# Performance work log

Measured on AMD Instinct MI355X. Metric: run time of the kernel, lower is better.

The kernel has to match this reference:

```python
import jax, jax.numpy as jnp
import numpy as np

EPS = 1e-6

def _sigma(x):
    # ELU+1 feature map used by Infini-Attention / linear attention
    return jax.nn.elu(x) + 1.0

def setup_inputs() -> dict:
    key = jax.random.key(0)
    ks = jax.random.split(key, 8)
    B, S, H, D = 2, 4096, 2048, 128
    sc = 1.0 / np.sqrt(H)
    return {
        "hidden_states": jax.random.normal(ks[0], (B, S, H), jnp.float32),
        "w_q": jax.random.normal(ks[1], (D, H), jnp.float32) * sc,
        "w_k": jax.random.normal(ks[2], (D, H), jnp.float32) * sc,
        "w_v": jax.random.normal(ks[3], (D, H), jnp.float32) * sc,
        "w_o": jax.random.normal(ks[4], (H, D), jnp.float32) * (1.0 / np.sqrt(D)),
        "gate": jnp.zeros((1,), jnp.float32),
        "M": jax.random.normal(ks[5], (D, D), jnp.float32),
        "z": jax.random.uniform(ks[6], (D,), jnp.float32) + 0.5,
    }

def reference(hidden_states, w_q, w_k, w_v, w_o, gate, M, z):
    # projections (torch Linear: x @ W^T)
    q = jnp.einsum('bsh,dh->bsd', hidden_states, w_q)
    k = jnp.einsum('bsh,dh->bsd', hidden_states, w_k)
    v = jnp.einsum('bsh,dh->bsd', hidden_states, w_v)

    # --- compressive memory retrieve: sigma(q) M / (sigma(q) . z) ---
    sq = _sigma(q)                                   # [B,S,D]
    mem_num = jnp.einsum('bsd,de->bse', sq, M)       # [B,S,D]
    mem_den = jnp.einsum('bsd,d->bs', sq, z) + EPS
    memory_output = mem_num / mem_den[..., None]

    # --- causal linear attention (cumulative-sum, non-softmax) ---
    pq, pk = _sigma(q), _sigma(k)
    kv_cum = jnp.cumsum(jnp.einsum('bsd,bse->bsde', pk, v), axis=1)  # [B,S,D,D] running state
    k_cum = jnp.cumsum(pk, axis=1)                                    # [B,S,D]
    num = jnp.einsum('bsd,bsde->bse', pq, kv_cum)
    den = jnp.einsum('bsd,bsd->bs', pq, k_cum) + EPS
    local_output = num / den[..., None]

    g = jax.nn.sigmoid(gate)                         # [1], broadcasts
    output = g * memory_output + (1.0 - g) * local_output

    # --- delta-rule memory update ---
    sk = _sigma(k)
    v_ret = jnp.einsum('bsd,de->bse', sk, M) / (jnp.einsum('bsd,d->bs', sk, z) + EPS)[..., None]
    M_new = M + jnp.einsum('bsd,bse->de', sk, v - v_ret)
    z_new = z + jnp.sum(sk, axis=(0, 1))

    out = jnp.einsum('bsd,hd->bsh', output, w_o)
    return out, M_new, z_new
```

## Files before the change

kernel.cpp:

```cpp
#include <hip/hip_runtime.h>
#include <hip/hip_bf16.h>
#include <math.h>

#define DI __device__ __forceinline__

typedef __bf16 bf16x8 __attribute__((ext_vector_type(8)));
typedef float  f32x4  __attribute__((ext_vector_type(4)));

static constexpr int   Bsz  = 2, Ssz = 4096, Hsz = 2048, Dsz = 128;
static constexpr int   Nrow = Bsz * Ssz;
static constexpr int   NCH  = Nrow / 128;
static constexpr int   CPB  = Ssz / 128;
static constexpr int   WN   = Dsz * Hsz;
static constexpr float EPSF = 1e-6f;

static constexpr size_t WQKV_OFF = 0;
static constexpr size_t WO_OFF   = (size_t)3*WN*2;
static constexpr size_t MB_OFF   = WO_OFF + (size_t)WN*2;
static constexpr size_t MBT_OFF  = MB_OFF + 32768;
static constexpr size_t QB_OFF   = MBT_OFF + 32768;
static constexpr size_t KB_OFF   = QB_OFF + (size_t)Nrow*Dsz*2;
static constexpr size_t VB_OFF   = KB_OFF + (size_t)Nrow*Dsz*2;
static constexpr size_t PB_OFF   = VB_OFF + (size_t)Nrow*Dsz*2;
static constexpr size_t ACC_OFF  = PB_OFF + (size_t)Nrow*Dsz*2;
static constexpr size_t KVT_OFF  = ACC_OFF;
static constexpr size_t KVTP_OFF = ACC_OFF + (size_t)4*1024*1024;
static constexpr size_t MPART_OFF= ACC_OFF + (size_t)6*1024*1024;
static constexpr size_t KSUM_OFF = ACC_OFF + (size_t)10*1024*1024;
static constexpr size_t KPRE_OFF = KSUM_OFF + 32768;

DI float b2f(unsigned short u) {
    union { float f; unsigned int i; } x; x.i = ((unsigned int)u) << 16; return x.f;
}
DI unsigned short f2b(float f) {
    __bf16 h = (__bf16)f; return __builtin_bit_cast(unsigned short, h);
}
DI float sig_elu(float x) { return x > 0.f ? x + 1.f : expf(x); }

DI f32x4 MFMA(bf16x8 a, bf16x8 b, f32x4 c) {
    return __builtin_amdgcn_mfma_f32_16x16x32_bf16(a, b, c, 0, 0, 0);
}
template<int NB>
DI void zaccg(f32x4 (&acc)[4][NB]) {
    f32x4 zz = {0.f, 0.f, 0.f, 0.f};
    #pragma unroll
    for (int i = 0; i < 4; i++)
        #pragma unroll
        for (int j = 0; j < NB; j++) acc[i][j] = zz;
}

DI int swzR(int r, int kc, int R) { return (kc*R + (r ^ (kc & 7))) * 8; }

template<int NKS, int NB>
DI void mmg(const unsigned short* A, const unsigned short* Bm, f32x4 (&acc)[4][NB],
            int wm, int wn, int quad, int lr) {
    #pragma unroll
    for (int ks = 0; ks < NKS; ks++) {
        bf16x8 a[4], b[NB];
        #pragma unroll
        for (int mb = 0; mb < 4; mb++)
            a[mb] = *(const bf16x8*)&A[swzR(wm*64 + mb*16 + lr, ks*4 + quad, 128)];
        #pragma unroll
        for (int nb = 0; nb < NB; nb++)
            b[nb] = *(const bf16x8*)&Bm[swzR(wn*(NB*16) + nb*16 + lr, ks*4 + quad, NB*32)];
        #pragma unroll
        for (int mb = 0; mb < 4; mb++)
            #pragma unroll
            for (int nb = 0; nb < NB; nb++)
                acc[mb][nb] = MFMA(a[mb], b[nb], acc[mb][nb]);
    }
}

template<int R>
DI void stage_dir(unsigned short* dst, const unsigned short* src, int src_ld, int tid) {
    #pragma unroll
    for (int i = 0; i < R/16; i++) {
        int s = tid + i*256; int r = s >> 4, kc = s & 15;
        *(uint4*)&dst[swzR(r, kc, R)] = *(const uint4*)(src + (size_t)r*src_ld + kc*8);
    }
}

DI void stage_T128(unsigned short* dst, const unsigned short* src, int src_ld, int tid) {
    #pragma unroll
    for (int i = 0; i < 8; i++) {
        int s = tid + i*256;
        int rw = (s & 15) + ((s >> 8) << 4);
        int c0 = ((s >> 4) & 15) * 8;
        unsigned short tmp[8];
        *(uint4*)tmp = *(const uint4*)(src + (size_t)rw*src_ld + c0);
        #pragma unroll
        for (int j = 0; j < 8; j++)
            dst[swzR(c0 + j, rw >> 3, 128) + (rw & 7)] = tmp[j];
    }
}

DI void stage_T64(unsigned short* dst, const unsigned short* src, int src_ld, int colOff, int tid) {
    #pragma unroll
    for (int i = 0; i < 4; i++) {
        int s = tid + i*256;
        int rw = (s & 15) + ((s >> 7) << 4);
        int c0 = ((s >> 4) & 7) * 8;
        unsigned short tmp[8];
        *(uint4*)tmp = *(const uint4*)(src + (size_t)rw*src_ld + colOff + c0);
        #pragma unroll
        for (int j = 0; j < 8; j++)
            dst[swzR(c0 + j, rw >> 3, 64) + (rw & 7)] = tmp[j];
    }
}


__global__ void k_cvt_w(const float* __restrict__ wq, const float* __restrict__ wk,
                        const float* __restrict__ wv, const float* __restrict__ wo,
                        const float* __restrict__ M, unsigned short* __restrict__ dst,
                        unsigned short* __restrict__ MbT)
{
    int gid = blockIdx.x*256 + threadIdx.x;
    if (gid >= (4*WN + 16384)/4) return;
    int e = gid*4;
    const float* src; int rel;
    if      (e < WN)     { src = wq; rel = e; }
    else if (e < 2*WN)   { src = wk; rel = e - WN; }
    else if (e < 3*WN)   { src = wv; rel = e - 2*WN; }
    else if (e < 4*WN)   { src = wo; rel = e - 3*WN; }
    else                 { src = M;  rel = e - 4*WN; }
    float4 v = *(const float4*)(src + rel);
    const float* vf = (const float*)&v;
    unsigned short o[4];
    #pragma unroll
    for (int j = 0; j < 4; j++) o[j] = f2b(vf[j]);
    *(uint2*)&dst[e] = *(const uint2*)o;
    if (e >= 4*WN) {
        #pragma unroll
        for (int j = 0; j < 4; j++) {
            int d = (rel + j) >> 7, ee = (rel + j) & 127;
            MbT[ee*128 + d] = o[j];
        }
    }
}

__global__ __launch_bounds__(256, 3) void k_gemm_qkv(
    const float* __restrict__ X, const unsigned short* __restrict__ W,
    unsigned short* __restrict__ AccB)
{
    __shared__ unsigned short lA[128*64];
    __shared__ unsigned short lB[128*64];
    const int tid = threadIdx.x;
    const int row0 = blockIdx.x * 128;
    const int ct   = blockIdx.y;
    const int n0   = ct * 128;
    const int kb   = blockIdx.z * 512;
    const int wave = tid >> 6, lane = tid & 63;
    const int wm = wave >> 1, wn = wave & 1;
    const int quad = lane >> 4, lr = lane & 15;

    f32x4 acc[4][4]; zaccg(acc);

    for (int kt = kb; kt < kb + 512; kt += 64) {
        #pragma unroll
        for (int i = 0; i < 4; i++) {
            int s = tid + i*256; int r = s >> 3, kc = s & 7;
            const float* gp = X + (size_t)(row0 + r)*Hsz + kt + kc*8;
            float4 a0 = *(const float4*)gp;
            float4 a1 = *(const float4*)(gp + 4);
            const float* f0 = (const float*)&a0;
            const float* f1 = (const float*)&a1;
            unsigned short tmp[8];
            #pragma unroll
            for (int j = 0; j < 4; j++) { tmp[j] = f2b(f0[j]); tmp[4+j] = f2b(f1[j]); }
            *(uint4*)&lA[swzR(r, kc, 128)] = *(const uint4*)tmp;
        }
        #pragma unroll
        for (int i = 0; i < 4; i++) {
            int s = tid + i*256; int r = s >> 3, kc = s & 7;
            *(uint4*)&lB[swzR(r, kc, 128)] = *(const uint4*)(W + (size_t)(n0 + r)*Hsz + kt + kc*8);
        }
        __syncthreads();
        mmg<2,4>(lA, lB, acc, wm, wn, quad, lr);
        __syncthreads();
    }

    unsigned short* base = AccB + ((size_t)(blockIdx.z*3 + ct))*Nrow*128;
    #pragma unroll
    for (int mb = 0; mb < 4; mb++)
        #pragma unroll
        for (int nb = 0; nb < 4; nb++)
            #pragma unroll
            for (int rg = 0; rg < 4; rg++) {
                int s_ = wm*64 + mb*16 + quad*4 + rg;
                int e_ = wn*64 + nb*16 + lr;
                base[(size_t)(row0 + s_)*128 + e_] = f2b(acc[mb][nb][rg]);
            }
}

__global__ void k_qkv_epi(const unsigned short* __restrict__ AccB,
                          unsigned short* __restrict__ Qb,
                          unsigned short* __restrict__ Kb, unsigned short* __restrict__ Vb)
{
    int gid = blockIdx.x*256 + threadIdx.x;
    int ct = gid / (Nrow*16);
    int off = (gid - ct*Nrow*16) * 8;
    float vs[8];
    #pragma unroll
    for (int j = 0; j < 8; j++) vs[j] = 0.f;
    #pragma unroll
    for (int s = 0; s < 4; s++) {
        uint4 u = *(const uint4*)&AccB[((size_t)s*3 + ct)*Nrow*128 + off];
        const unsigned short* us = (const unsigned short*)&u;
        #pragma unroll
        for (int j = 0; j < 8; j++) vs[j] += b2f(us[j]);
    }
    unsigned short o[8];
    if (ct < 2) {
        #pragma unroll
        for (int j = 0; j < 8; j++) o[j] = f2b(sig_elu(vs[j]));
    } else {
        #pragma unroll
        for (int j = 0; j < 8; j++) o[j] = f2b(vs[j]);
    }
    unsigned short* dst = (ct == 0) ? Qb : (ct == 1 ? Kb : Vb);
    *(uint4*)&dst[off] = *(const uint4*)o;
}

__global__ __launch_bounds__(256, 1) void k_delta_kv(
    const unsigned short* __restrict__ Kb, const unsigned short* __restrict__ Vb,
    const unsigned short* __restrict__ MbT, const float* __restrict__ z,
    float* __restrict__ KVT, float* __restrict__ ksum, float* __restrict__ Mpart)
{
    __shared__ unsigned short b0[128*128];
    __shared__ unsigned short b1[64*128];
    __shared__ float den[128];
    const int tid = threadIdx.x;
    const int c = blockIdx.x, t0 = c*128;
    const int h = blockIdx.y, e0 = h*64;
    const int wave = tid >> 6, lane = tid & 63;
    const int wm = wave >> 1, wn = wave & 1, quad = lane >> 4, lr = lane & 15;

    stage_dir<128>(b0, Kb + (size_t)t0*Dsz, Dsz, tid);
    stage_dir<64>(b1, MbT + (size_t)e0*128, 128, tid);
    __syncthreads();

    f32x4 acc1[4][2]; zaccg(acc1);
    mmg<4,2>(b0, b1, acc1, wm, wn, quad, lr);

    if (tid < 128) {
        float p = 0.f;
        for (int d = 0; d < 128; d++)
            p += b2f(b0[swzR(tid, d >> 3, 128) + (d & 7)]) * z[d];
        den[tid] = p + EPSF;
    }
    __syncthreads();

    stage_T128(b0, Kb + (size_t)t0*Dsz, Dsz, tid);
    #pragma unroll
    for (int mb = 0; mb < 4; mb++)
        #pragma unroll
        for (int nb = 0; nb < 2; nb++)
            #pragma unroll
            for (int rg = 0; rg < 4; rg++) {
                int s_ = wm*64 + mb*16 + quad*4 + rg;
                int el = wn*32 + nb*16 + lr;
                float v = b2f(Vb[(size_t)(t0 + s_)*Dsz + e0 + el]);
                float w = v - acc1[mb][nb][rg] / den[s_];
                b1[swzR(el, s_ >> 3, 64) + (s_ & 7)] = f2b(w);
            }
    __syncthreads();

    if (h == 0 && tid < 128) {
        float p = 0.f;
        for (int t = 0; t < 128; t++)
            p += b2f(b0[swzR(tid, t >> 3, 128) + (t & 7)]);
        ksum[(size_t)c*128 + tid] = p;
    }
    f32x4 acc2[4][2]; zaccg(acc2);
    mmg<4,2>(b0, b1, acc2, wm, wn, quad, lr);
    #pragma unroll
    for (int mb = 0; mb < 4; mb++)
        #pragma unroll
        for (int nb = 0; nb < 2; nb++)
            #pragma unroll
            for (int rg = 0; rg < 4; rg++) {
                int d_ = wm*64 + mb*16 + quad*4 + rg;
                int el = wn*32 + nb*16 + lr;
                Mpart[(size_t)c*16384 + (size_t)d_*128 + e0 + el] = acc2[mb][nb][rg];
            }
    __syncthreads();

    stage_T128(b0, Vb + (size_t)t0*Dsz, Dsz, tid);
    stage_T64(b1, Kb + (size_t)t0*Dsz, Dsz, e0, tid);
    __syncthreads();

    f32x4 acc3[4][2]; zaccg(acc3);
    mmg<4,2>(b0, b1, acc3, wm, wn, quad, lr);
    #pragma unroll
    for (int mb = 0; mb < 4; mb++)
        #pragma unroll
        for (int nb = 0; nb < 2; nb++)
            #pragma unroll
            for (int rg = 0; rg < 4; rg++) {
                int e_ = wm*64 + mb*16 + quad*4 + rg;
                int dl_ = wn*32 + nb*16 + lr;
                KVT[(size_t)c*16384 + (size_t)e_*128 + e0 + dl_] = acc3[mb][nb][rg];
            }
}

__global__ void k_scan_final(
    const float* __restrict__ KVT, const float* __restrict__ ksum,
    const float* __restrict__ M, const float* __restrict__ z,
    const float* __restrict__ Mpart, unsigned short* __restrict__ KVTp,
    float* __restrict__ kpre, float* __restrict__ omz)
{
    int idx = blockIdx.x*256 + threadIdx.x;
    if (idx < 32768) {
        int batch = idx >> 14, ed = idx & 16383;
        float a = 0.f;
        #pragma unroll 8
        for (int i = 0; i < CPB; i++) {
            size_t cc = (size_t)(batch*CPB + i);
            KVTp[cc*16384 + ed] = f2b(a);
            a += KVT[cc*16384 + ed];
        }
    } else if (idx < 33024) {
        int j = idx - 32768; int batch = j >> 7, d = j & 127;
        float a = 0.f;
        #pragma unroll 8
        for (int i = 0; i < CPB; i++) {
            int cc = batch*CPB + i;
            kpre[cc*128 + d] = a;
            a += ksum[cc*128 + d];
        }
    } else if (idx < 49408) {
        int m = idx - 33024;
        float a = M[m];
        #pragma unroll 8
        for (int cc = 0; cc < NCH; cc++) a += Mpart[(size_t)cc*16384 + m];
        omz[m] = a;
    } else if (idx < 49536) {
        int d = idx - 49408;
        float a = z[d];
        #pragma unroll 8
        for (int cc = 0; cc < NCH; cc++) a += ksum[cc*128 + d];
        omz[16384 + d] = a;
    }
}

__global__ __launch_bounds__(256, 1) void k_attn(
    const unsigned short* __restrict__ Qb, const unsigned short* __restrict__ KVTp,
    const float* __restrict__ kpre, const unsigned short* __restrict__ MbT,
    const float* __restrict__ z, const float* __restrict__ gate,
    const unsigned short* __restrict__ Kb, const unsigned short* __restrict__ Vb,
    unsigned short* __restrict__ P)
{
    __shared__ unsigned short b0[128*128];
    __shared__ unsigned short b1[128*128];
    __shared__ float dmem[128], dl[128], rs[128];
    const int tid = threadIdx.x;
    const int c = blockIdx.x, t0 = c*128;
    const int h = blockIdx.y, e0 = h*64;
    const int wave = tid >> 6, lane = tid & 63;
    const int wm = wave >> 1, wn = wave & 1, quad = lane >> 4, lr = lane & 15;
    unsigned short* b1lo = b1;
    unsigned short* b1hi = b1 + 64*128;

    if (tid < 128) rs[tid] = 0.f;
    stage_dir<128>(b0, Qb + (size_t)t0*Dsz, Dsz, tid);
    stage_dir<64>(b1lo, MbT + (size_t)e0*128, 128, tid);
    stage_dir<64>(b1hi, KVTp + (size_t)c*16384 + (size_t)e0*128, 128, tid);
    __syncthreads();

    if (tid < 128) {
        float p = 0.f;
        for (int d = 0; d < 128; d++)
            p += b2f(b0[swzR(tid, d >> 3, 128) + (d & 7)]) * z[d];
        dmem[tid] = p + EPSF;
    } else {
        int s_ = tid - 128; float p = 0.f;
        for (int d = 0; d < 128; d++)
            p += b2f(b0[swzR(s_, d >> 3, 128) + (d & 7)]) * kpre[c*128 + d];
        dl[s_] = p;
    }
    f32x4 accM[4][2]; zaccg(accM);
    mmg<4,2>(b0, b1lo, accM, wm, wn, quad, lr);
    f32x4 accN[4][2]; zaccg(accN);
    mmg<4,2>(b0, b1hi, accN, wm, wn, quad, lr);
    __syncthreads();

    float g = 1.f / (1.f + expf(-gate[0]));
    f32x4 base[4][2];
    #pragma unroll
    for (int mb = 0; mb < 4; mb++)
        #pragma unroll
        for (int nb = 0; nb < 2; nb++)
            #pragma unroll
            for (int rg = 0; rg < 4; rg++) {
                int s_ = wm*64 + mb*16 + quad*4 + rg;
                base[mb][nb][rg] = g * accM[mb][nb][rg] / dmem[s_];
            }
    stage_dir<128>(b1, Kb + (size_t)t0*Dsz, Dsz, tid);
    __syncthreads();

    f32x4 accS[4][4]; zaccg(accS);
    mmg<4,4>(b0, b1, accS, wm, wn, quad, lr);
    __syncthreads();

    #pragma unroll
    for (int mb = 0; mb < 4; mb++)
        #pragma unroll
        for (int rg = 0; rg < 4; rg++) {
            int s_ = wm*64 + mb*16 + quad*4 + rg;
            float part = 0.f;
            #pragma unroll
            for (int nb = 0; nb < 4; nb++) {
                int t_ = wn*64 + nb*16 + lr;
                float v = (t_ <= s_) ? accS[mb][nb][rg] : 0.f;
                part += v;
                b0[swzR(s_, t_ >> 3, 128) + (t_ & 7)] = f2b(v);
            }
            #pragma unroll
            for (int m = 1; m < 16; m <<= 1) part += __shfl_xor(part, m, 64);
            if (lr == 0) atomicAdd(&rs[s_], part);
        }
    stage_T64(b1lo, Vb + (size_t)t0*Dsz, Dsz, e0, tid);
    __syncthreads();

    f32x4 accV[4][2]; zaccg(accV);
    mmg<4,2>(b0, b1lo, accV, wm, wn, quad, lr);

    #pragma unroll
    for (int mb = 0; mb < 4; mb++)
        #pragma unroll
        for (int nb = 0; nb < 2; nb++)
            #pragma unroll
            for (int rg = 0; rg < 4; rg++) {
                int s_ = wm*64 + mb*16 + quad*4 + rg;
                int el = wn*32 + nb*16 + lr;
                float num = accN[mb][nb][rg] + accV[mb][nb][rg];
                float dd  = dl[s_] + rs[s_] + EPSF;
                float val = base[mb][nb][rg] + (1.f - g) * num / dd;
                P[(size_t)(t0 + s_)*Dsz + e0 + el] = f2b(val);
            }
}

__global__ __launch_bounds__(256, 2) void k_gemm_out(
    const unsigned short* __restrict__ P, const unsigned short* __restrict__ Wo,
    float* __restrict__ out)
{
    __shared__ unsigned short b0[128*128];
    __shared__ unsigned short b1[128*128];
    const int tid = threadIdx.x;
    const int row0 = blockIdx.x*128, n0 = blockIdx.y*128;
    const int wave = tid >> 6, lane = tid & 63;
    const int wm = wave >> 1, wn = wave & 1, quad = lane >> 4, lr = lane & 15;

    stage_dir<128>(b0, P  + (size_t)row0*Dsz, Dsz, tid);
    stage_dir<128>(b1, Wo + (size_t)n0*Dsz,  Dsz, tid);
    __syncthreads();

    f32x4 acc[4][4]; zaccg(acc);
    mmg<4,4>(b0, b1, acc, wm, wn, quad, lr);
    #pragma unroll
    for (int mb = 0; mb < 4; mb++)
        #pragma unroll
        for (int nb = 0; nb < 4; nb++)
            #pragma unroll
            for (int rg = 0; rg < 4; rg++) {
                int s_ = wm*64 + mb*16 + quad*4 + rg;
                int e_ = wn*64 + nb*16 + lr;
                out[(size_t)(row0 + s_)*Hsz + n0 + e_] = acc[mb][nb][rg];
            }
}

extern "C" void kernel_launch(void* const* d_in, const int* in_sizes, int n_in,
                              void* d_out, int out_size, void* d_ws, size_t ws_size,
                              hipStream_t stream)
{
    const float* X    = (const float*)d_in[0];
    const float* wq   = (const float*)d_in[1];
    const float* wk   = (const float*)d_in[2];
    const float* wv   = (const float*)d_in[3];
    const float* wo   = (const float*)d_in[4];
    const float* gate = (const float*)d_in[5];
    const float* M    = (const float*)d_in[6];
    const float* z    = (const float*)d_in[7];

    char* ws = (char*)d_ws;
    unsigned short* Wfull = (unsigned short*)(ws + WQKV_OFF);
    unsigned short* Wo_b  = (unsigned short*)(ws + WO_OFF);
    unsigned short* MbT   = (unsigned short*)(ws + MBT_OFF);
    unsigned short* Qb    = (unsigned short*)(ws + QB_OFF);
    unsigned short* Kb    = (unsigned short*)(ws + KB_OFF);
    unsigned short* Vb    = (unsigned short*)(ws + VB_OFF);
    unsigned short* Pb    = (unsigned short*)(ws + PB_OFF);
    unsigned short* AccB  = (unsigned short*)(ws + ACC_OFF);
    float* KVT   = (float*)(ws + KVT_OFF);
    unsigned short* KVTp = (unsigned short*)(ws + KVTP_OFF);
    float* Mpart = (float*)(ws + MPART_OFF);
    float* ksum  = (float*)(ws + KSUM_OFF);
    float* kpre  = (float*)(ws + KPRE_OFF);

    float* outp   = (float*)d_out;
    float* out_mz = outp + (size_t)Nrow*Hsz;

    k_cvt_w<<<((4*WN + 16384)/4 + 255)/256, 256, 0, stream>>>(wq, wk, wv, wo, M, Wfull, MbT);
    k_gemm_qkv<<<dim3(Nrow/128, 3, 4), 256, 0, stream>>>(X, Wfull, AccB);
    k_qkv_epi<<<(3*Nrow*16)/256, 256, 0, stream>>>(AccB, Qb, Kb, Vb);
    k_delta_kv<<<dim3(NCH, 2), 256, 0, stream>>>(Kb, Vb, MbT, z, KVT, ksum, Mpart);
    k_scan_final<<<194, 256, 0, stream>>>(KVT, ksum, M, z, Mpart, KVTp, kpre, out_mz);
    k_attn<<<dim3(NCH, 2), 256, 0, stream>>>(Qb, KVTp, kpre, MbT, z, gate, Kb, Vb, Pb);
    k_gemm_out<<<dim3(Nrow/128, Hsz/128), 256, 0, stream>>>(Pb, Wo_b, outp);
}
```

Before: 207.8 us.

## Use direct global-to-LDS loads in GEMMs and split delta/attn kernels across more blocks

The QKV and output GEMMs now stage tiles with global_load_lds straight into XOR-swizzled shared memory. In the QKV GEMM the fp32 activations are kept in LDS and converted to bf16 at fragment-read time, replacing the register round-trip and conversion during staging. The delta-rule and attention kernels split the value dimension into 32-wide slices (4 y-blocks instead of 2), raise occupancy bounds, and store the KV state untransposed so that KV and Mpart share one epilogue. Holding fp32 tiles doubles LDS use for the A operand, and the finer split re-stages the K and Q tiles more times.

```diff
diff --git a/kernel.cpp b/kernel.cpp
--- a/kernel.cpp
+++ b/kernel.cpp
@@ -23,8 +23,8 @@
 static constexpr size_t VB_OFF   = KB_OFF + (size_t)Nrow*Dsz*2;
 static constexpr size_t PB_OFF   = VB_OFF + (size_t)Nrow*Dsz*2;
 static constexpr size_t ACC_OFF  = PB_OFF + (size_t)Nrow*Dsz*2;
-static constexpr size_t KVT_OFF  = ACC_OFF;
-static constexpr size_t KVTP_OFF = ACC_OFF + (size_t)4*1024*1024;
+static constexpr size_t KV_OFF   = ACC_OFF;
+static constexpr size_t KVP_OFF  = ACC_OFF + (size_t)4*1024*1024;
 static constexpr size_t MPART_OFF= ACC_OFF + (size_t)6*1024*1024;
 static constexpr size_t KSUM_OFF = ACC_OFF + (size_t)10*1024*1024;
 static constexpr size_t KPRE_OFF = KSUM_OFF + 32768;
@@ -47,6 +47,11 @@
     for (int i = 0; i < 4; i++)
         #pragma unroll
         for (int j = 0; j < NB; j++) acc[i][j] = zz;
+}
+
+DI void gll16(const void* g, void* l) {
+    __builtin_amdgcn_global_load_lds((const __attribute__((address_space(1))) void*)g,
+                                     (__attribute__((address_space(3))) void*)l, 16, 0, 0);
 }
 
 DI int swzR(int r, int kc, int R) { return (kc*R + (r ^ (kc & 7))) * 8; }
@@ -94,17 +99,17 @@
     }
 }
 
-DI void stage_T64(unsigned short* dst, const unsigned short* src, int src_ld, int colOff, int tid) {
-    #pragma unroll
-    for (int i = 0; i < 4; i++) {
+DI void stage_T32(unsigned short* dst, const unsigned short* src, int src_ld, int colOff, int tid) {
+    #pragma unroll
+    for (int i = 0; i < 2; i++) {
         int s = tid + i*256;
-        int rw = (s & 15) + ((s >> 7) << 4);
-        int c0 = ((s >> 4) & 7) * 8;
+        int rw = (s & 15) + ((s >> 6) << 4);
+        int c0 = ((s >> 4) & 3) * 8;
         unsigned short tmp[8];
         *(uint4*)tmp = *(const uint4*)(src + (size_t)rw*src_ld + colOff + c0);
         #pragma unroll
         for (int j = 0; j < 8; j++)
-            dst[swzR(c0 + j, rw >> 3, 64) + (rw & 7)] = tmp[j];
+            dst[swzR(c0 + j, rw >> 3, 32) + (rw & 7)] = tmp[j];
     }
 }
 
@@ -142,7 +147,7 @@
     const float* __restrict__ X, const unsigned short* __restrict__ W,
     unsigned short* __restrict__ AccB)
 {
-    __shared__ unsigned short lA[128*64];
+    __shared__ float          lA[128*64];
     __shared__ unsigned short lB[128*64];
     const int tid = threadIdx.x;
     const int row0 = blockIdx.x * 128;
@@ -157,25 +162,42 @@
 
     for (int kt = kb; kt < kb + 512; kt += 64) {
         #pragma unroll
+        for (int i = 0; i < 8; i++) {
+            int p = tid + i*256; int r = p >> 4; int kc = (p & 15) ^ (r & 15);
+            gll16(X + (size_t)(row0 + r)*Hsz + kt + kc*4, &lA[p*4]);
+        }
+        #pragma unroll
         for (int i = 0; i < 4; i++) {
-            int s = tid + i*256; int r = s >> 3, kc = s & 7;
-            const float* gp = X + (size_t)(row0 + r)*Hsz + kt + kc*8;
-            float4 a0 = *(const float4*)gp;
-            float4 a1 = *(const float4*)(gp + 4);
-            const float* f0 = (const float*)&a0;
-            const float* f1 = (const float*)&a1;
-            unsigned short tmp[8];
-            #pragma unroll
-            for (int j = 0; j < 4; j++) { tmp[j] = f2b(f0[j]); tmp[4+j] = f2b(f1[j]); }
-            *(uint4*)&lA[swzR(r, kc, 128)] = *(const uint4*)tmp;
-        }
-        #pragma unroll
-        for (int i = 0; i < 4; i++) {
-            int s = tid + i*256; int r = s >> 3, kc = s & 7;
-            *(uint4*)&lB[swzR(r, kc, 128)] = *(const uint4*)(W + (size_t)(n0 + r)*Hsz + kt + kc*8);
+            int p = tid + i*256; int r = p >> 3; int kc = (p & 7) ^ (r & 7);
+            gll16(W + (size_t)(n0 + r)*Hsz + kt + kc*8, &lB[p*8]);
         }
         __syncthreads();
-        mmg<2,4>(lA, lB, acc, wm, wn, quad, lr);
+        #pragma unroll
+        for (int ks = 0; ks < 2; ks++) {
+            bf16x8 a[4], b[4];
+            #pragma unroll
+            for (int mb = 0; mb < 4; mb++) {
+                int r = wm*64 + mb*16 + lr;
+                int c0 = (ks*4 + quad)*2;
+                f32x4 u0 = *(const f32x4*)&lA[(r*16 + ( c0      ^ (r & 15)))*4];
+                f32x4 u1 = *(const f32x4*)&lA[(r*16 + ((c0 + 1) ^ (r & 15)))*4];
+                bf16x8 t;
+                #pragma unroll
+                for (int j = 0; j < 4; j++) { t[j] = (__bf16)u0[j]; t[4+j] = (__bf16)u1[j]; }
+                a[mb] = t;
+            }
+            #pragma unroll
+            for (int nb = 0; nb < 4; nb++) {
+                int r = wn*64 + nb*16 + lr;
+                int c = (ks*4 + quad) ^ (r & 7);
+                b[nb] = *(const bf16x8*)&lB[(r*8 + c)*8];
+            }
+            #pragma unroll
+            for (int mb = 0; mb < 4; mb++)
+                #pragma unroll
+                for (int nb = 0; nb < 4; nb++)
+                    acc[mb][nb] = MFMA(a[mb], b[nb], acc[mb][nb]);
+        }
         __syncthreads();
     }
 
@@ -221,26 +243,28 @@
     *(uint4*)&dst[off] = *(const uint4*)o;
 }
 
-__global__ __launch_bounds__(256, 1) void k_delta_kv(
+__global__ __launch_bounds__(256, 2) void k_delta_kv(
     const unsigned short* __restrict__ Kb, const unsigned short* __restrict__ Vb,
     const unsigned short* __restrict__ MbT, const float* __restrict__ z,
-    float* __restrict__ KVT, float* __restrict__ ksum, float* __restrict__ Mpart)
+    float* __restrict__ KV, float* __restrict__ ksum, float* __restrict__ Mpart)
 {
     __shared__ unsigned short b0[128*128];
-    __shared__ unsigned short b1[64*128];
+    __shared__ unsigned short b1a[32*128];
+    __shared__ unsigned short b1b[32*128];
+    __shared__ unsigned short b1c[32*128];
     __shared__ float den[128];
     const int tid = threadIdx.x;
     const int c = blockIdx.x, t0 = c*128;
-    const int h = blockIdx.y, e0 = h*64;
+    const int e0 = blockIdx.y * 32;
     const int wave = tid >> 6, lane = tid & 63;
     const int wm = wave >> 1, wn = wave & 1, quad = lane >> 4, lr = lane & 15;
 
     stage_dir<128>(b0, Kb + (size_t)t0*Dsz, Dsz, tid);
-    stage_dir<64>(b1, MbT + (size_t)e0*128, 128, tid);
-    __syncthreads();
-
-    f32x4 acc1[4][2]; zaccg(acc1);
-    mmg<4,2>(b0, b1, acc1, wm, wn, quad, lr);
+    stage_dir<32>(b1a, MbT + (size_t)e0*128, 128, tid);
+    __syncthreads();
+
+    f32x4 acc1[4][1]; zaccg(acc1);
+    mmg<4,1>(b0, b1a, acc1, wm, wn, quad, lr);
 
     if (tid < 128) {
         float p = 0.f;
@@ -251,62 +275,44 @@
     __syncthreads();
 
     stage_T128(b0, Kb + (size_t)t0*Dsz, Dsz, tid);
-    #pragma unroll
-    for (int mb = 0; mb < 4; mb++)
-        #pragma unroll
-        for (int nb = 0; nb < 2; nb++)
-            #pragma unroll
-            for (int rg = 0; rg < 4; rg++) {
-                int s_ = wm*64 + mb*16 + quad*4 + rg;
-                int el = wn*32 + nb*16 + lr;
-                float v = b2f(Vb[(size_t)(t0 + s_)*Dsz + e0 + el]);
-                float w = v - acc1[mb][nb][rg] / den[s_];
-                b1[swzR(el, s_ >> 3, 64) + (s_ & 7)] = f2b(w);
-            }
-    __syncthreads();
-
-    if (h == 0 && tid < 128) {
+    stage_T32(b1c, Vb + (size_t)t0*Dsz, Dsz, e0, tid);
+    #pragma unroll
+    for (int mb = 0; mb < 4; mb++)
+        #pragma unroll
+        for (int rg = 0; rg < 4; rg++) {
+            int s_ = wm*64 + mb*16 + quad*4 + rg;
+            int el = wn*16 + lr;
+            float v = b2f(Vb[(size_t)(t0 + s_)*Dsz + e0 + el]);
+            float w = v - acc1[mb][0][rg] / den[s_];
+            b1b[swzR(el, s_ >> 3, 32) + (s_ & 7)] = f2b(w);
+        }
+    __syncthreads();
+
+    if (e0 == 0 && tid < 128) {
         float p = 0.f;
         for (int t = 0; t < 128; t++)
             p += b2f(b0[swzR(tid, t >> 3, 128) + (t & 7)]);
         ksum[(size_t)c*128 + tid] = p;
     }
-    f32x4 acc2[4][2]; zaccg(acc2);
-    mmg<4,2>(b0, b1, acc2, wm, wn, quad, lr);
-    #pragma unroll
-    for (int mb = 0; mb < 4; mb++)
-        #pragma unroll
-        for (int nb = 0; nb < 2; nb++)
-            #pragma unroll
-            for (int rg = 0; rg < 4; rg++) {
-                int d_ = wm*64 + mb*16 + quad*4 + rg;
-                int el = wn*32 + nb*16 + lr;
-                Mpart[(size_t)c*16384 + (size_t)d_*128 + e0 + el] = acc2[mb][nb][rg];
-            }
-    __syncthreads();
-
-    stage_T128(b0, Vb + (size_t)t0*Dsz, Dsz, tid);
-    stage_T64(b1, Kb + (size_t)t0*Dsz, Dsz, e0, tid);
-    __syncthreads();
-
-    f32x4 acc3[4][2]; zaccg(acc3);
-    mmg<4,2>(b0, b1, acc3, wm, wn, quad, lr);
-    #pragma unroll
-    for (int mb = 0; mb < 4; mb++)
-        #pragma unroll
-        for (int nb = 0; nb < 2; nb++)
-            #pragma unroll
-            for (int rg = 0; rg < 4; rg++) {
-                int e_ = wm*64 + mb*16 + quad*4 + rg;
-                int dl_ = wn*32 + nb*16 + lr;
-                KVT[(size_t)c*16384 + (size_t)e_*128 + e0 + dl_] = acc3[mb][nb][rg];
-            }
+    f32x4 acc2[4][1]; zaccg(acc2);
+    mmg<4,1>(b0, b1b, acc2, wm, wn, quad, lr);
+    f32x4 acc3[4][1]; zaccg(acc3);
+    mmg<4,1>(b0, b1c, acc3, wm, wn, quad, lr);
+    #pragma unroll
+    for (int mb = 0; mb < 4; mb++)
+        #pragma unroll
+        for (int rg = 0; rg < 4; rg++) {
+            int d_ = wm*64 + mb*16 + quad*4 + rg;
+            int el = wn*16 + lr;
+            Mpart[(size_t)c*16384 + (size_t)d_*128 + e0 + el] = acc2[mb][0][rg];
+            KV[(size_t)c*16384 + (size_t)d_*128 + e0 + el]    = acc3[mb][0][rg];
+        }
 }
 
 __global__ void k_scan_final(
-    const float* __restrict__ KVT, const float* __restrict__ ksum,
+    const float* __restrict__ KV, const float* __restrict__ ksum,
     const float* __restrict__ M, const float* __restrict__ z,
-    const float* __restrict__ Mpart, unsigned short* __restrict__ KVTp,
+    const float* __restrict__ Mpart, unsigned short* __restrict__ KVp,
     float* __restrict__ kpre, float* __restrict__ omz)
 {
     int idx = blockIdx.x*256 + threadIdx.x;
@@ -316,8 +322,8 @@
         #pragma unroll 8
         for (int i = 0; i < CPB; i++) {
             size_t cc = (size_t)(batch*CPB + i);
-            KVTp[cc*16384 + ed] = f2b(a);
-            a += KVT[cc*16384 + ed];
+            KVp[cc*16384 + ed] = f2b(a);
+            a += KV[cc*16384 + ed];
         }
     } else if (idx < 33024) {
         int j = idx - 32768; int batch = j >> 7, d = j & 127;
@@ -343,8 +349,8 @@
     }
 }
 
-__global__ __launch_bounds__(256, 1) void k_attn(
-    const unsigned short* __restrict__ Qb, const unsigned short* __restrict__ KVTp,
+__global__ __launch_bounds__(256, 2) void k_attn(
+    const unsigned short* __restrict__ Qb, const unsigned short* __restrict__ KVp,
     const float* __restrict__ kpre, const unsigned short* __restrict__ MbT,
     const float* __restrict__ z, const float* __restrict__ gate,
     const unsigned short* __restrict__ Kb, const unsigned short* __restrict__ Vb,
@@ -355,16 +361,16 @@
     __shared__ float dmem[128], dl[128], rs[128];
     const int tid = threadIdx.x;
     const int c = blockIdx.x, t0 = c*128;
-    const int h = blockIdx.y, e0 = h*64;
+    const int e0 = blockIdx.y * 32;
     const int wave = tid >> 6, lane = tid & 63;
     const int wm = wave >> 1, wn = wave & 1, quad = lane >> 4, lr = lane & 15;
-    unsigned short* b1lo = b1;
-    unsigned short* b1hi = b1 + 64*128;
+    unsigned short* b1q0 = b1;
+    unsigned short* b1q1 = b1 + 32*128;
 
     if (tid < 128) rs[tid] = 0.f;
     stage_dir<128>(b0, Qb + (size_t)t0*Dsz, Dsz, tid);
-    stage_dir<64>(b1lo, MbT + (size_t)e0*128, 128, tid);
-    stage_dir<64>(b1hi, KVTp + (size_t)c*16384 + (size_t)e0*128, 128, tid);
+    stage_dir<32>(b1q0, MbT + (size_t)e0*128, 128, tid);
+    stage_T32(b1q1, KVp + (size_t)c*16384, 128, e0, tid);
     __syncthreads();
 
     if (tid < 128) {
@@ -378,23 +384,21 @@
             p += b2f(b0[swzR(s_, d >> 3, 128) + (d & 7)]) * kpre[c*128 + d];
         dl[s_] = p;
     }
-    f32x4 accM[4][2]; zaccg(accM);
-    mmg<4,2>(b0, b1lo, accM, wm, wn, quad, lr);
-    f32x4 accN[4][2]; zaccg(accN);
-    mmg<4,2>(b0, b1hi, accN, wm, wn, quad, lr);
+    f32x4 accM[4][1]; zaccg(accM);
+    mmg<4,1>(b0, b1q0, accM, wm, wn, quad, lr);
+    f32x4 accN[4][1]; zaccg(accN);
+    mmg<4,1>(b0, b1q1, accN, wm, wn, quad, lr);
     __syncthreads();
 
     float g = 1.f / (1.f + expf(-gate[0]));
-    f32x4 base[4][2];
-    #pragma unroll
-    for (int mb = 0; mb < 4; mb++)
-        #pragma unroll
-        for (int nb = 0; nb < 2; nb++)
-            #pragma unroll
-            for (int rg = 0; rg < 4; rg++) {
-                int s_ = wm*64 + mb*16 + quad*4 + rg;
-                base[mb][nb][rg] = g * accM[mb][nb][rg] / dmem[s_];
-            }
+    f32x4 base[4][1];
+    #pragma unroll
+    for (int mb = 0; mb < 4; mb++)
+        #pragma unroll
+        for (int rg = 0; rg < 4; rg++) {
+            int s_ = wm*64 + mb*16 + quad*4 + rg;
+            base[mb][0][rg] = g * accM[mb][0][rg] / dmem[s_];
+        }
     stage_dir<128>(b1, Kb + (size_t)t0*Dsz, Dsz, tid);
     __syncthreads();
 
@@ -419,25 +423,23 @@
             for (int m = 1; m < 16; m <<= 1) part += __shfl_xor(part, m, 64);
             if (lr == 0) atomicAdd(&rs[s_], part);
         }
-    stage_T64(b1lo, Vb + (size_t)t0*Dsz, Dsz, e0, tid);
-    __syncthreads();
-
-    f32x4 accV[4][2]; zaccg(accV);
-    mmg<4,2>(b0, b1lo, accV, wm, wn, quad, lr);
-
-    #pragma unroll
-    for (int mb = 0; mb < 4; mb++)
-        #pragma unroll
-        for (int nb = 0; nb < 2; nb++)
-            #pragma unroll
-            for (int rg = 0; rg < 4; rg++) {
-                int s_ = wm*64 + mb*16 + quad*4 + rg;
-                int el = wn*32 + nb*16 + lr;
-                float num = accN[mb][nb][rg] + accV[mb][nb][rg];
-                float dd  = dl[s_] + rs[s_] + EPSF;
-                float val = base[mb][nb][rg] + (1.f - g) * num / dd;
-                P[(size_t)(t0 + s_)*Dsz + e0 + el] = f2b(val);
-            }
+    stage_T32(b1q0, Vb + (size_t)t0*Dsz, Dsz, e0, tid);
+    __syncthreads();
+
+    f32x4 accV[4][1]; zaccg(accV);
+    mmg<4,1>(b0, b1q0, accV, wm, wn, quad, lr);
+
+    #pragma unroll
+    for (int mb = 0; mb < 4; mb++)
+        #pragma unroll
+        for (int rg = 0; rg < 4; rg++) {
+            int s_ = wm*64 + mb*16 + quad*4 + rg;
+            int el = wn*16 + lr;
+            float num = accN[mb][0][rg] + accV[mb][0][rg];
+            float dd  = dl[s_] + rs[s_] + EPSF;
+            float val = base[mb][0][rg] + (1.f - g) * num / dd;
+            P[(size_t)(t0 + s_)*Dsz + e0 + el] = f2b(val);
+        }
 }
 
 __global__ __launch_bounds__(256, 2) void k_gemm_out(
@@ -451,12 +453,38 @@
     const int wave = tid >> 6, lane = tid & 63;
     const int wm = wave >> 1, wn = wave & 1, quad = lane >> 4, lr = lane & 15;
 
-    stage_dir<128>(b0, P  + (size_t)row0*Dsz, Dsz, tid);
-    stage_dir<128>(b1, Wo + (size_t)n0*Dsz,  Dsz, tid);
+    #pragma unroll
+    for (int i = 0; i < 8; i++) {
+        int p = tid + i*256; int r = p >> 4; int kc = (p & 15) ^ (r & 15);
+        gll16(P + (size_t)(row0 + r)*Dsz + kc*8, &b0[p*8]);
+    }
+    #pragma unroll
+    for (int i = 0; i < 8; i++) {
+        int p = tid + i*256; int r = p >> 4; int kc = (p & 15) ^ (r & 15);
+        gll16(Wo + (size_t)(n0 + r)*Dsz + kc*8, &b1[p*8]);
+    }
     __syncthreads();
 
     f32x4 acc[4][4]; zaccg(acc);
-    mmg<4,4>(b0, b1, acc, wm, wn, quad, lr);
+    #pragma unroll
+    for (int ks = 0; ks < 4; ks++) {
+        bf16x8 a[4], b[4];
+        #pragma unroll
+        for (int mb = 0; mb < 4; mb++) {
+            int r = wm*64 + mb*16 + lr;
+            a[mb] = *(const bf16x8*)&b0[(r*16 + ((ks*4 + quad) ^ (r & 15)))*8];
+        }
+        #pragma unroll
+        for (int nb = 0; nb < 4; nb++) {
+            int r = wn*64 + nb*16 + lr;
+            b[nb] = *(const bf16x8*)&b1[(r*16 + ((ks*4 + quad) ^ (r & 15)))*8];
+        }
+        #pragma unroll
+        for (int mb = 0; mb < 4; mb++)
+            #pragma unroll
+            for (int nb = 0; nb < 4; nb++)
+                acc[mb][nb] = MFMA(a[mb], b[nb], acc[mb][nb]);
+    }
     #pragma unroll
     for (int mb = 0; mb < 4; mb++)
         #pragma unroll
@@ -491,8 +519,8 @@
     unsigned short* Vb    = (unsigned short*)(ws + VB_OFF);
     unsigned short* Pb    = (unsigned short*)(ws + PB_OFF);
     unsigned short* AccB  = (unsigned short*)(ws + ACC_OFF);
-    float* KVT   = (float*)(ws + KVT_OFF);
-    unsigned short* KVTp = (unsigned short*)(ws + KVTP_OFF);
+    float* KV    = (float*)(ws + KV_OFF);
+    unsigned short* KVp = (unsigned short*)(ws + KVP_OFF);
     float* Mpart = (float*)(ws + MPART_OFF);
     float* ksum  = (float*)(ws + KSUM_OFF);
     float* kpre  = (float*)(ws + KPRE_OFF);
@@ -503,8 +531,8 @@
     k_cvt_w<<<((4*WN + 16384)/4 + 255)/256, 256, 0, stream>>>(wq, wk, wv, wo, M, Wfull, MbT);
     k_gemm_qkv<<<dim3(Nrow/128, 3, 4), 256, 0, stream>>>(X, Wfull, AccB);
     k_qkv_epi<<<(3*Nrow*16)/256, 256, 0, stream>>>(AccB, Qb, Kb, Vb);
-    k_delta_kv<<<dim3(NCH, 2), 256, 0, stream>>>(Kb, Vb, MbT, z, KVT, ksum, Mpart);
-    k_scan_final<<<194, 256, 0, stream>>>(KVT, ksum, M, z, Mpart, KVTp, kpre, out_mz);
-    k_attn<<<dim3(NCH, 2), 256, 0, stream>>>(Qb, KVTp, kpre, MbT, z, gate, Kb, Vb, Pb);
+    k_delta_kv<<<dim3(NCH, 4), 256, 0, stream>>>(Kb, Vb, MbT, z, KV, ksum, Mpart);
+    k_scan_final<<<194, 256, 0, stream>>>(KV, ksum, M, z, Mpart, KVp, kpre, out_mz);
+    k_attn<<<dim3(NCH, 4), 256, 0, stream>>>(Qb, KVp, kpre, MbT, z, gate, Kb, Vb, Pb);
     k_gemm_out<<<dim3(Nrow/128, Hsz/128), 256, 0, stream>>>(Pb, Wo_b, outp);
 }
```

New measurement: 188.9 us. -9.1%, faster.
